# Performance work log

Hardware: AMD Instinct MI355X
Metric: run time of the kernel (lower is better)

Reference implementation:

```python
import jax, jax.numpy as jnp
import numpy as np

B, H, S, D = 4, 8, 4096, 64

def setup_inputs() -> dict:
    key = jax.random.key(0)
    kq, kk, kv = jax.random.split(key, 3)
    Q = jax.random.normal(kq, (B, H, S, D), dtype=jnp.float32)
    K = jax.random.normal(kk, (B, H, S, D), dtype=jnp.float32)
    V = jax.random.normal(kv, (B, H, S, D), dtype=jnp.float32)
    return {"Q": Q, "K": K, "V": V}

def reference(Q, K, V):
    scale = 1.0 / jnp.sqrt(jnp.float32(Q.shape[-1]))
    # scores: [B, H, S, S]
    scores = jnp.einsum('bhqd,bhkd->bhqk', Q, K) * scale
    attn = jax.nn.softmax(scores, axis=-1)
    # out: [B, H, S, D]
    return jnp.einsum('bhqk,bhkd->bhqd', attn, V)
```

## Files before the change

kernel.cpp:

```cpp
#include <hip/hip_runtime.h>
#include <hip/hip_bf16.h>

typedef float  f32x16 __attribute__((ext_vector_type(16)));
typedef __bf16 bf16x8 __attribute__((ext_vector_type(8)));
typedef __bf16 bf16x4 __attribute__((ext_vector_type(4)));
typedef __bf16 bf16x2 __attribute__((ext_vector_type(2)));
typedef int    i32x2v __attribute__((ext_vector_type(2)));
typedef int    i32x4v __attribute__((ext_vector_type(4)));

#define SEQ   4096
#define DDIM  64
#define KB    64
#define NT    (SEQ / KB)
#define TILEB 16384
#define WSNEED (32ull * NT * TILEB)
#define SCL   0.18033688011112042f
#define DEFT  16.0f

#if __has_builtin(__builtin_amdgcn_exp2f)
#define EXP2(x) __builtin_amdgcn_exp2f(x)
#else
#define EXP2(x) __expf((x) * 0.6931471805599453f)
#endif

__device__ __forceinline__ int swzb(int row) {
  return (row & 7) ^ ((row >> 3) & 3);
}

__device__ __forceinline__ void pswap32(int &x, int &y) {
#if __has_builtin(__builtin_amdgcn_permlane32_swap)
  i32x2v r = __builtin_amdgcn_permlane32_swap(x, y, false, false);
  x = r[0]; y = r[1];
#else
  asm volatile("v_permlane32_swap_b32 %0, %1" : "+v"(x), "+v"(y));
#endif
}

__device__ __forceinline__ void mfma_acc(f32x16 &acc, bf16x8 a, bf16x8 b) {
  asm("v_mfma_f32_32x32x16_bf16 %0, %1, %2, %0"
      : "+v"(acc) : "v"(a), "v"(b));
}
__device__ __forceinline__ f32x16 mfma_z(bf16x8 a, bf16x8 b) {
  f32x16 d;
  asm("v_mfma_f32_32x32x16_bf16 %0, %1, %2, 0"
      : "=v"(d) : "v"(a), "v"(b));
  return d;
}

__device__ __forceinline__ void gl_lds16(const char* g, char* l) {
  __builtin_amdgcn_global_load_lds(
      (const __attribute__((address_space(1))) void*)g,
      (__attribute__((address_space(3))) void*)l, 16, 0, 0);
}

__device__ __forceinline__ bf16x8 mkfrag(int a, int b, int c, int d) {
  i32x4v v; v[0] = a; v[1] = b; v[2] = c; v[3] = d;
  return __builtin_bit_cast(bf16x8, v);
}

__device__ __forceinline__ float max8(const f32x16& s, int o) {
  float m = fmaxf(fmaxf(s[o+0], s[o+1]), s[o+2]);
  m = fmaxf(fmaxf(m, s[o+3]), s[o+4]);
  m = fmaxf(fmaxf(m, s[o+5]), s[o+6]);
  return fmaxf(m, s[o+7]);
}

__global__ __launch_bounds__(256)
void prep(const float* __restrict__ Kg, const float* __restrict__ Vg,
          char* __restrict__ KVb)
{
  int i = blockIdx.x * 256 + threadIdx.x;
  if (i < (1 << 20)) {
    int row = i >> 3, s_in = i & 7;
    int bh = row >> 12, r = row & 4095, t = r >> 6, kv = r & 63;
    const float* src = Kg + (size_t)row * 64 + s_in * 8;
    float4 f0 = *(const float4*)(src);
    float4 f1 = *(const float4*)(src + 4);
    bf16x8 p;
    p[0] = (__bf16)f0.x; p[1] = (__bf16)f0.y; p[2] = (__bf16)f0.z; p[3] = (__bf16)f0.w;
    p[4] = (__bf16)f1.x; p[5] = (__bf16)f1.y; p[6] = (__bf16)f1.z; p[7] = (__bf16)f1.w;
    char* dst = KVb + (size_t)(bh * NT + t) * TILEB + kv * 128 + ((s_in ^ swzb(kv)) * 16);
    *(bf16x8*)dst = p;
  } else {
    int j = i - (1 << 20);
    int d = j & 63, rest = j >> 6;
    int kvg = rest & 7, t = (rest >> 3) & 63, bh = rest >> 9;
    const float* src = Vg + (size_t)bh * (SEQ * DDIM) + (t * 64 + kvg * 8) * 64 + d;
    bf16x8 p;
    #pragma unroll
    for (int jj = 0; jj < 8; ++jj) p[jj] = (__bf16)src[jj * 64];
    char* dst = KVb + (size_t)(bh * NT + t) * TILEB + 8192 + d * 128
              + ((kvg ^ swzb(d)) * 16);
    *(bf16x8*)dst = p;
  }
}

__global__ __launch_bounds__(512, 4)
void fattn(const float* __restrict__ Qg, const char* __restrict__ KVb,
           float* __restrict__ Og)
{
  __shared__ __align__(16) char smem[3 * TILEB];

  const int tid  = threadIdx.x;
  const int w    = tid >> 6;
  const int lane = tid & 63;
  const int q31  = lane & 31;
  const int h    = lane >> 5;

  int wg = (int)blockIdx.x;
  wg = (wg & 7) * 64 + (wg >> 3);
  const int bh = wg >> 4;
  const int qb = wg & 15;
  const size_t base = (size_t)bh * (SEQ * DDIM);
  const int qrow = qb * 256 + w * 32 + q31;

  bf16x8 aq[4];
  {
    const float* qp = Qg + base + (size_t)qrow * DDIM + 8 * h;
    #pragma unroll
    for (int c = 0; c < 4; ++c) {
      float4 f0 = *(const float4*)(qp + 16 * c);
      float4 f1 = *(const float4*)(qp + 16 * c + 4);
      aq[c][0] = (__bf16)(f0.x * SCL);
      aq[c][1] = (__bf16)(f0.y * SCL);
      aq[c][2] = (__bf16)(f0.z * SCL);
      aq[c][3] = (__bf16)(f0.w * SCL);
      aq[c][4] = (__bf16)(f1.x * SCL);
      aq[c][5] = (__bf16)(f1.y * SCL);
      aq[c][6] = (__bf16)(f1.z * SCL);
      aq[c][7] = (__bf16)(f1.w * SCL);
    }
  }

  const char* kvt = KVb + (size_t)bh * (NT * TILEB);
  const int stg   = w * 1024 + lane * 16;
  const int ldsw  = w * 1024;

  const int swr = swzb(q31) << 4;
  int kaddr[4];
  #pragma unroll
  for (int c = 0; c < 4; ++c)
    kaddr[c] = q31 * 128 + ((32 * c + 16 * h) ^ swr);

  f32x16 o0 = {}, o1 = {};
  float lsum = 0.f;
  int pk[2][8];

#if __has_builtin(__builtin_amdgcn_fdot2_f32_bf16)
  bf16x2 one2; one2[0] = (__bf16)1.0f; one2[1] = (__bf16)1.0f;
#endif

  auto softmax_pack = [&](f32x16& s0, f32x16& s1) {
    #pragma unroll
    for (int r = 0; r < 16; ++r) s0[r] = EXP2(s0[r]);
    #pragma unroll
    for (int r = 0; r < 16; ++r) s1[r] = EXP2(s1[r]);
    #pragma unroll
    for (int u = 0; u < 8; ++u) {
      bf16x2 p0; p0[0] = (__bf16)s0[2*u]; p0[1] = (__bf16)s0[2*u+1];
      pk[0][u] = __builtin_bit_cast(int, p0);
      bf16x2 p1; p1[0] = (__bf16)s1[2*u]; p1[1] = (__bf16)s1[2*u+1];
      pk[1][u] = __builtin_bit_cast(int, p1);
    }
#if __has_builtin(__builtin_amdgcn_fdot2_f32_bf16)
    float a0 = 0.f, a1 = 0.f, a2 = 0.f, a3 = 0.f;
    #pragma unroll
    for (int u = 0; u < 2; ++u) {
      a0 = __builtin_amdgcn_fdot2_f32_bf16(__builtin_bit_cast(bf16x2, pk[0][4*u+0]), one2, a0, false);
      a1 = __builtin_amdgcn_fdot2_f32_bf16(__builtin_bit_cast(bf16x2, pk[0][4*u+1]), one2, a1, false);
      a2 = __builtin_amdgcn_fdot2_f32_bf16(__builtin_bit_cast(bf16x2, pk[0][4*u+2]), one2, a2, false);
      a3 = __builtin_amdgcn_fdot2_f32_bf16(__builtin_bit_cast(bf16x2, pk[0][4*u+3]), one2, a3, false);
      a0 = __builtin_amdgcn_fdot2_f32_bf16(__builtin_bit_cast(bf16x2, pk[1][4*u+0]), one2, a0, false);
      a1 = __builtin_amdgcn_fdot2_f32_bf16(__builtin_bit_cast(bf16x2, pk[1][4*u+1]), one2, a1, false);
      a2 = __builtin_amdgcn_fdot2_f32_bf16(__builtin_bit_cast(bf16x2, pk[1][4*u+2]), one2, a2, false);
      a3 = __builtin_amdgcn_fdot2_f32_bf16(__builtin_bit_cast(bf16x2, pk[1][4*u+3]), one2, a3, false);
    }
    lsum += (a0 + a1) + (a2 + a3);
#else
    f32x16 ts = s0 + s1;
    lsum += ((((ts[0]+ts[1])+(ts[2]+ts[3])) + ((ts[4]+ts[5])+(ts[6]+ts[7])))
          +  (((ts[8]+ts[9])+(ts[10]+ts[11])) + ((ts[12]+ts[13])+(ts[14]+ts[15]))));
#endif
    #pragma unroll
    for (int m = 0; m < 2; ++m) {
      pswap32(pk[m][0], pk[m][2]);
      pswap32(pk[m][1], pk[m][3]);
      pswap32(pk[m][4], pk[m][6]);
      pswap32(pk[m][5], pk[m][7]);
    }
  };

  {
    const char* gp = kvt + stg;
    gl_lds16(gp,                smem + ldsw);
    gl_lds16(gp + 8192,         smem + ldsw + 8192);
    gl_lds16(gp + TILEB,        smem + TILEB + ldsw);
    gl_lds16(gp + TILEB + 8192, smem + TILEB + ldsw + 8192);
  }
  asm volatile("s_waitcnt vmcnt(2)" ::: "memory");
  __builtin_amdgcn_s_barrier();

  int b0 = 0, b1 = TILEB, b2 = 2 * TILEB;

  for (int t = 0; t < NT; ++t) {
    const bool issue2 = (t + 2) < NT;

    if (issue2) {
      const char* gp = kvt + (size_t)(t + 2) * TILEB + stg;
      gl_lds16(gp,        smem + b2 + ldsw);
      gl_lds16(gp + 8192, smem + b2 + ldsw + 8192);
    }

    f32x16 s0, s1;
    __builtin_amdgcn_s_setprio(1);
    {
      bf16x8 k0 = *(const bf16x8*)(smem + b0 + kaddr[0]);
      bf16x8 k1 = *(const bf16x8*)(smem + b0 + kaddr[0] + 4096);
      s0 = mfma_z(k0, aq[0]);
      s1 = mfma_z(k1, aq[0]);
    }
    #pragma unroll
    for (int c = 1; c < 4; ++c) {
      bf16x8 k0 = *(const bf16x8*)(smem + b0 + kaddr[c]);
      bf16x8 k1 = *(const bf16x8*)(smem + b0 + kaddr[c] + 4096);
      mfma_acc(s0, k0, aq[c]);
      mfma_acc(s1, k1, aq[c]);
    }
    __builtin_amdgcn_s_setprio(0);

    softmax_pack(s0, s1);

    __builtin_amdgcn_s_setprio(1);
    #pragma unroll
    for (int c = 0; c < 4; ++c) {
      bf16x8 bp = mkfrag(pk[c>>1][(c&1)*4+0], pk[c>>1][(c&1)*4+1],
                         pk[c>>1][(c&1)*4+2], pk[c>>1][(c&1)*4+3]);
      bf16x8 v0 = *(const bf16x8*)(smem + b0 + kaddr[c] + 8192);
      bf16x8 v1 = *(const bf16x8*)(smem + b0 + kaddr[c] + 12288);
      mfma_acc(o0, v0, bp);
      mfma_acc(o1, v1, bp);
    }
    __builtin_amdgcn_s_setprio(0);

    if (t + 1 < NT) {
      if (issue2) asm volatile("s_waitcnt vmcnt(2)" ::: "memory");
      else        asm volatile("s_waitcnt vmcnt(0)" ::: "memory");
      __builtin_amdgcn_s_barrier();
    }
    int tmp = b0; b0 = b1; b1 = b2; b2 = tmp;
  }

  float l = lsum + __shfl_xor(lsum, 32);
  float inv = 1.0f / l;
  float* op = Og + base + (size_t)qrow * DDIM + 4 * h;
  #pragma unroll
  for (int rg = 0; rg < 4; ++rg) {
    float4 st0 = { o0[4*rg+0]*inv, o0[4*rg+1]*inv, o0[4*rg+2]*inv, o0[4*rg+3]*inv };
    *(float4*)(op + 8*rg) = st0;
    float4 st1 = { o1[4*rg+0]*inv, o1[4*rg+1]*inv, o1[4*rg+2]*inv, o1[4*rg+3]*inv };
    *(float4*)(op + 8*rg + 32) = st1;
  }
}

__global__ __launch_bounds__(512)
void fattn_fb(const float* __restrict__ Qg, const float* __restrict__ Kg,
              const float* __restrict__ Vg, float* __restrict__ Og)
{
  __shared__ __align__(16) char smem[32768];
  const int tid  = threadIdx.x;
  const int w    = tid >> 6;
  const int lane = tid & 63;
  const int q31  = lane & 31;
  const int h    = lane >> 5;

  int wg = (int)blockIdx.x;
  wg = (wg & 7) * 64 + (wg >> 3);
  const int bh = wg >> 4;
  const int qb = wg & 15;
  const size_t base = (size_t)bh * (SEQ * DDIM);
  const int qrow = qb * 256 + w * 32 + q31;

  bf16x8 aq[4];
  {
    const float* qp = Qg + base + (size_t)qrow * DDIM + 8 * h;
    #pragma unroll
    for (int c = 0; c < 4; ++c) {
      float4 f0 = *(const float4*)(qp + 16 * c);
      float4 f1 = *(const float4*)(qp + 16 * c + 4);
      aq[c][0] = (__bf16)(f0.x * SCL); aq[c][1] = (__bf16)(f0.y * SCL);
      aq[c][2] = (__bf16)(f0.z * SCL); aq[c][3] = (__bf16)(f0.w * SCL);
      aq[c][4] = (__bf16)(f1.x * SCL); aq[c][5] = (__bf16)(f1.y * SCL);
      aq[c][6] = (__bf16)(f1.z * SCL); aq[c][7] = (__bf16)(f1.w * SCL);
    }
  }

  const int kvA = tid >> 4;
  const int dK  = (tid & 15) * 4;
  const int kw0 = ((kvA * 128 + dK * 2) ^ (swzb(kvA) << 4));
  const int kv0 = (tid >> 4) * 2;
  const int dV  = (tid & 15) * 4;
  int vw[4];
  #pragma unroll
  for (int qq = 0; qq < 4; ++qq)
    vw[qq] = 8192 + (((dV + qq) * 128 + kv0 * 2) ^ (swzb(dV + qq) << 4));
  const float* kptr = Kg + base + (size_t)kvA * DDIM + dK;
  const float* vptr = Vg + base + (size_t)kv0 * DDIM + dV;

  const int swr = swzb(q31) << 4;
  int kaddr[4];
  #pragma unroll
  for (int c = 0; c < 4; ++c)
    kaddr[c] = q31 * 128 + ((32 * c + 16 * h) ^ swr);

  f32x16 o0 = {}, o1 = {};
  float mrow = 0.f, lsum = 0.f;

  {
    float4 ka = *(const float4*)(kptr);
    float4 kb = *(const float4*)(kptr + 32 * DDIM);
    float4 va = *(const float4*)(vptr);
    float4 vb = *(const float4*)(vptr + DDIM);
    bf16x4 pa, pb;
    pa[0]=(__bf16)ka.x; pa[1]=(__bf16)ka.y; pa[2]=(__bf16)ka.z; pa[3]=(__bf16)ka.w;
    pb[0]=(__bf16)kb.x; pb[1]=(__bf16)kb.y; pb[2]=(__bf16)kb.z; pb[3]=(__bf16)kb.w;
    *(bf16x4*)(smem + kw0)            = pa;
    *(bf16x4*)(smem + kw0 + 32 * 128) = pb;
    float va4[4] = {va.x, va.y, va.z, va.w};
    float vb4[4] = {vb.x, vb.y, vb.z, vb.w};
    #pragma unroll
    for (int qq = 0; qq < 4; ++qq) {
      bf16x2 p; p[0] = (__bf16)va4[qq]; p[1] = (__bf16)vb4[qq];
      *(bf16x2*)(smem + vw[qq]) = p;
    }
  }

  int rbase = 0;
  for (int t = 0; t < NT; ++t) {
    __syncthreads();
    const bool more = (t + 1) < NT;
    const float* kpt = kptr + (size_t)(t + 1) * (KB * DDIM);
    const float* vpt = vptr + (size_t)(t + 1) * (KB * DDIM);
    float4 ka = {}, kb = {};
    if (more) { ka = *(const float4*)(kpt); kb = *(const float4*)(kpt + 32 * DDIM); }

    f32x16 s0 = {}, s1 = {};
    #pragma unroll
    for (int c = 0; c < 4; ++c) {
      bf16x8 k0 = *(const bf16x8*)(smem + rbase + kaddr[c]);
      bf16x8 k1 = *(const bf16x8*)(smem + rbase + kaddr[c] + 4096);
      s0 = __builtin_amdgcn_mfma_f32_32x32x16_bf16(k0, aq[c], s0, 0, 0, 0);
      s1 = __builtin_amdgcn_mfma_f32_32x32x16_bf16(k1, aq[c], s1, 0, 0, 0);
    }

    float4 va = {}, vb = {};
    if (more) { va = *(const float4*)(vpt); vb = *(const float4*)(vpt + DDIM); }

    float pm;
    {
      float m0 = max8(s0, 0), m1 = max8(s0, 8);
      float m2 = max8(s1, 0), m3 = max8(s1, 8);
      pm = fmaxf(fmaxf(m0, m1), fmaxf(m2, m3));
    }
    if (!__all(pm <= mrow + DEFT)) {
      float tm = fmaxf(pm, __shfl_xor(pm, 32));
      float mn = fmaxf(mrow, tm);
      float corr = EXP2(mrow - mn);
      o0 *= corr; o1 *= corr; lsum *= corr;
      mrow = mn;
    }
    #pragma unroll
    for (int r = 0; r < 16; ++r) s0[r] = EXP2(s0[r] - mrow);
    #pragma unroll
    for (int r = 0; r < 16; ++r) s1[r] = EXP2(s1[r] - mrow);
    f32x16 ts = s0 + s1;
    lsum += ((((ts[0]+ts[1])+(ts[2]+ts[3])) + ((ts[4]+ts[5])+(ts[6]+ts[7])))
          +  (((ts[8]+ts[9])+(ts[10]+ts[11])) + ((ts[12]+ts[13])+(ts[14]+ts[15]))));

    int pk[2][8];
    #pragma unroll
    for (int u = 0; u < 8; ++u) {
      bf16x2 p0; p0[0] = (__bf16)s0[2*u]; p0[1] = (__bf16)s0[2*u+1];
      pk[0][u] = __builtin_bit_cast(int, p0);
      bf16x2 p1; p1[0] = (__bf16)s1[2*u]; p1[1] = (__bf16)s1[2*u+1];
      pk[1][u] = __builtin_bit_cast(int, p1);
    }
    #pragma unroll
    for (int m = 0; m < 2; ++m) {
      pswap32(pk[m][0], pk[m][2]); pswap32(pk[m][1], pk[m][3]);
      pswap32(pk[m][4], pk[m][6]); pswap32(pk[m][5], pk[m][7]);
    }

    const int wb = rbase ^ 16384;
    if (more) {
      bf16x4 pa, pb;
      pa[0]=(__bf16)ka.x; pa[1]=(__bf16)ka.y; pa[2]=(__bf16)ka.z; pa[3]=(__bf16)ka.w;
      pb[0]=(__bf16)kb.x; pb[1]=(__bf16)kb.y; pb[2]=(__bf16)kb.z; pb[3]=(__bf16)kb.w;
      *(bf16x4*)(smem + wb + kw0)            = pa;
      *(bf16x4*)(smem + wb + kw0 + 32 * 128) = pb;
    }

    #pragma unroll
    for (int c = 0; c < 4; ++c) {
      bf16x8 bp = mkfrag(pk[c>>1][(c&1)*4+0], pk[c>>1][(c&1)*4+1],
                         pk[c>>1][(c&1)*4+2], pk[c>>1][(c&1)*4+3]);
      bf16x8 v0 = *(const bf16x8*)(smem + rbase + kaddr[c] + 8192);
      bf16x8 v1 = *(const bf16x8*)(smem + rbase + kaddr[c] + 12288);
      o0 = __builtin_amdgcn_mfma_f32_32x32x16_bf16(v0, bp, o0, 0, 0, 0);
      o1 = __builtin_amdgcn_mfma_f32_32x32x16_bf16(v1, bp, o1, 0, 0, 0);
    }

    if (more) {
      float va4[4] = {va.x, va.y, va.z, va.w};
      float vb4[4] = {vb.x, vb.y, vb.z, vb.w};
      #pragma unroll
      for (int qq = 0; qq < 4; ++qq) {
        bf16x2 p; p[0] = (__bf16)va4[qq]; p[1] = (__bf16)vb4[qq];
        *(bf16x2*)(smem + wb + vw[qq]) = p;
      }
    }
    rbase ^= 16384;
  }

  float l = lsum + __shfl_xor(lsum, 32);
  float inv = 1.0f / l;
  float* op = Og + base + (size_t)qrow * DDIM + 4 * h;
  #pragma unroll
  for (int rg = 0; rg < 4; ++rg) {
    float4 w0 = { o0[4*rg+0]*inv, o0[4*rg+1]*inv, o0[4*rg+2]*inv, o0[4*rg+3]*inv };
    *(float4*)(op + 8*rg) = w0;
    float4 w1 = { o1[4*rg+0]*inv, o1[4*rg+1]*inv, o1[4*rg+2]*inv, o1[4*rg+3]*inv };
    *(float4*)(op + 8*rg + 32) = w1;
  }
}

extern "C" void kernel_launch(void* const* d_in, const int* in_sizes, int n_in,
                              void* d_out, int out_size, void* d_ws, size_t ws_size,
                              hipStream_t stream) {
  const float* Q = (const float*)d_in[0];
  const float* K = (const float*)d_in[1];
  const float* V = (const float*)d_in[2];
  float* O = (float*)d_out;
  if (ws_size >= WSNEED) {
    prep<<<dim3(8192), dim3(256), 0, stream>>>(K, V, (char*)d_ws);
    fattn<<<dim3(512), dim3(512), 0, stream>>>(Q, (const char*)d_ws, O);
  } else {
    fattn_fb<<<dim3(512), dim3(512), 0, stream>>>(Q, K, V, O);
  }
}
```

Measured before the change: 157.4 us.

## Restructure K/V pipeline into double-buffered tile pairs with one barrier per pair

Replaces the three-slot rotating LDS ring, which had one barrier per KV tile, with a four-tile LDS layout organised as two double-buffered pairs. Each pair of tiles gets a single barrier, and both next-pair loads are issued during compute on the current pair. This halves barrier and waitcnt synchronisation. In exchange, LDS per block grows from 48KB to 64KB, which may limit occupancy under the launch bounds, and the wait before each barrier is now a full vmcnt(0) drain.

```diff
diff --git a/kernel.cpp b/kernel.cpp
--- a/kernel.cpp
+++ b/kernel.cpp
@@ -99,7 +99,7 @@
 void fattn(const float* __restrict__ Qg, const char* __restrict__ KVb,
            float* __restrict__ Og)
 {
-  __shared__ __align__(16) char smem[3 * TILEB];
+  __shared__ __align__(16) char smem[4 * TILEB];
 
   const int tid  = threadIdx.x;
   const int w    = tid >> 6;
@@ -190,6 +190,39 @@
     }
   };
 
+  auto tile_compute = [&](int b) {
+    f32x16 s0, s1;
+    __builtin_amdgcn_s_setprio(1);
+    {
+      bf16x8 k0 = *(const bf16x8*)(smem + b + kaddr[0]);
+      bf16x8 k1 = *(const bf16x8*)(smem + b + kaddr[0] + 4096);
+      s0 = mfma_z(k0, aq[0]);
+      s1 = mfma_z(k1, aq[0]);
+    }
+    #pragma unroll
+    for (int c = 1; c < 4; ++c) {
+      bf16x8 k0 = *(const bf16x8*)(smem + b + kaddr[c]);
+      bf16x8 k1 = *(const bf16x8*)(smem + b + kaddr[c] + 4096);
+      mfma_acc(s0, k0, aq[c]);
+      mfma_acc(s1, k1, aq[c]);
+    }
+    __builtin_amdgcn_s_setprio(0);
+
+    softmax_pack(s0, s1);
+
+    __builtin_amdgcn_s_setprio(1);
+    #pragma unroll
+    for (int c = 0; c < 4; ++c) {
+      bf16x8 bp = mkfrag(pk[c>>1][(c&1)*4+0], pk[c>>1][(c&1)*4+1],
+                         pk[c>>1][(c&1)*4+2], pk[c>>1][(c&1)*4+3]);
+      bf16x8 v0 = *(const bf16x8*)(smem + b + kaddr[c] + 8192);
+      bf16x8 v1 = *(const bf16x8*)(smem + b + kaddr[c] + 12288);
+      mfma_acc(o0, v0, bp);
+      mfma_acc(o1, v1, bp);
+    }
+    __builtin_amdgcn_s_setprio(0);
+  };
+
   {
     const char* gp = kvt + stg;
     gl_lds16(gp,                smem + ldsw);
@@ -197,57 +230,35 @@
     gl_lds16(gp + TILEB,        smem + TILEB + ldsw);
     gl_lds16(gp + TILEB + 8192, smem + TILEB + ldsw + 8192);
   }
-  asm volatile("s_waitcnt vmcnt(2)" ::: "memory");
+  asm volatile("s_waitcnt vmcnt(0)" ::: "memory");
   __builtin_amdgcn_s_barrier();
 
-  int b0 = 0, b1 = TILEB, b2 = 2 * TILEB;
-
-  for (int t = 0; t < NT; ++t) {
-    const bool issue2 = (t + 2) < NT;
-
-    if (issue2) {
-      const char* gp = kvt + (size_t)(t + 2) * TILEB + stg;
-      gl_lds16(gp,        smem + b2 + ldsw);
-      gl_lds16(gp + 8192, smem + b2 + ldsw + 8192);
-    }
-
-    f32x16 s0, s1;
-    __builtin_amdgcn_s_setprio(1);
-    {
-      bf16x8 k0 = *(const bf16x8*)(smem + b0 + kaddr[0]);
-      bf16x8 k1 = *(const bf16x8*)(smem + b0 + kaddr[0] + 4096);
-      s0 = mfma_z(k0, aq[0]);
-      s1 = mfma_z(k1, aq[0]);
-    }
-    #pragma unroll
-    for (int c = 1; c < 4; ++c) {
-      bf16x8 k0 = *(const bf16x8*)(smem + b0 + kaddr[c]);
-      bf16x8 k1 = *(const bf16x8*)(smem + b0 + kaddr[c] + 4096);
-      mfma_acc(s0, k0, aq[c]);
-      mfma_acc(s1, k1, aq[c]);
-    }
-    __builtin_amdgcn_s_setprio(0);
-
-    softmax_pack(s0, s1);
-
-    __builtin_amdgcn_s_setprio(1);
-    #pragma unroll
-    for (int c = 0; c < 4; ++c) {
-      bf16x8 bp = mkfrag(pk[c>>1][(c&1)*4+0], pk[c>>1][(c&1)*4+1],
-                         pk[c>>1][(c&1)*4+2], pk[c>>1][(c&1)*4+3]);
-      bf16x8 v0 = *(const bf16x8*)(smem + b0 + kaddr[c] + 8192);
-      bf16x8 v1 = *(const bf16x8*)(smem + b0 + kaddr[c] + 12288);
-      mfma_acc(o0, v0, bp);
-      mfma_acc(o1, v1, bp);
-    }
-    __builtin_amdgcn_s_setprio(0);
-
-    if (t + 1 < NT) {
-      if (issue2) asm volatile("s_waitcnt vmcnt(2)" ::: "memory");
-      else        asm volatile("s_waitcnt vmcnt(0)" ::: "memory");
+  for (int p = 0; p < NT / 2; ++p) {
+    const int cur = (p & 1) << 15;
+    const int nxt = cur ^ 32768;
+    const int t0 = 2 * p;
+    const bool morep = (p + 1) < (NT / 2);
+
+    if (morep) {
+      const char* gp = kvt + (size_t)(t0 + 2) * TILEB + stg;
+      gl_lds16(gp,        smem + nxt + ldsw);
+      gl_lds16(gp + 8192, smem + nxt + ldsw + 8192);
+    }
+
+    tile_compute(cur);
+
+    if (morep) {
+      const char* gp = kvt + (size_t)(t0 + 3) * TILEB + stg;
+      gl_lds16(gp,        smem + nxt + TILEB + ldsw);
+      gl_lds16(gp + 8192, smem + nxt + TILEB + ldsw + 8192);
+    }
+
+    tile_compute(cur + TILEB);
+
+    if (morep) {
+      asm volatile("s_waitcnt vmcnt(0)" ::: "memory");
       __builtin_amdgcn_s_barrier();
     }
-    int tmp = b0; b0 = b1; b1 = b2; b2 = tmp;
   }
 
   float l = lsum + __shfl_xor(lsum, 32);
```

Result: slower. 161.8 us (+2.9%).
